# Kernel optimization log

Hardware: AMD Instinct MI355X
Metric: run time of the kernel (lower is better)

## Reference

```python
import jax, jax.numpy as jnp
import numpy as np

B, N, D, E, L = 8, 4096, 256, 65536, 1  # graphs, padded nodes, d_model, padded edges, num_layers


def setup_inputs() -> dict:
    key = jax.random.key(0)
    ks = jax.random.split(key, 9)
    x = jax.random.normal(ks[0], (B, N, D), dtype=jnp.float32)
    edge_index = jax.random.randint(ks[1], (B, 2, E), 0, N)
    edge_weight = jax.random.uniform(ks[2], (B, E), dtype=jnp.float32)
    mask = jax.random.randint(ks[3], (B, N), 0, 2).astype(jnp.int32)
    s = 1.0 / np.sqrt(D)
    # GatedGraphConv per-layer linear weight [L, D, D]
    W = jax.random.uniform(ks[4], (L, D, D), jnp.float32, -s, s)
    # GRUCell parameters (r, z, n stacked)
    W_ih = jax.random.uniform(ks[5], (3 * D, D), jnp.float32, -s, s)
    W_hh = jax.random.uniform(ks[6], (3 * D, D), jnp.float32, -s, s)
    b_ih = jax.random.uniform(ks[7], (3 * D,), jnp.float32, -s, s)
    b_hh = jax.random.uniform(ks[8], (3 * D,), jnp.float32, -s, s)
    return {"x": x, "edge_index": edge_index, "edge_weight": edge_weight,
            "mask": mask, "W": W, "W_ih": W_ih, "W_hh": W_hh,
            "b_ih": b_ih, "b_hh": b_hh}


def _gated_graph_conv(x, u, v, ew, W, W_ih, W_hh, b_ih, b_hh):
    """x:[B,N,D]; u,v:[B,E] src/dst indices; ew:[B,E] (already masked)."""
    h = x
    for l in range(L):
        m = jnp.einsum('bnd,de->bne', h, W[l])            # linear transform
        msg = jnp.take_along_axis(m, u[..., None], axis=1) * ew[..., None]  # [B,E,D]
        agg = jax.vmap(lambda ms, vi: jax.ops.segment_sum(ms, vi, num_segments=N))(msg, v)
        # GRUCell(input=agg, hidden=h)
        gi = agg @ W_ih.T + b_ih                          # [B,N,3D]
        gh = h @ W_hh.T + b_hh
        r = jax.nn.sigmoid(gi[..., :D] + gh[..., :D])
        z = jax.nn.sigmoid(gi[..., D:2 * D] + gh[..., D:2 * D])
        n = jnp.tanh(gi[..., 2 * D:] + r * gh[..., 2 * D:])
        h = (1.0 - z) * n + z * h
    return h


def reference(x, edge_index, edge_weight, mask, W, W_ih, W_hh, b_ih, b_hh):
    node_valid = mask > 0                                  # [B,N]
    u = edge_index[:, 0]                                   # source
    v = edge_index[:, 1]                                   # target
    # Drop edges touching invalid nodes: weight -> 0 (equivalent under sum aggr)
    e_valid = jnp.take_along_axis(node_valid, u, axis=1) & jnp.take_along_axis(node_valid, v, axis=1)
    ew = edge_weight * e_valid.astype(edge_weight.dtype)
    h = _gated_graph_conv(x, u, v, ew, W, W_ih, W_hh, b_ih, b_hh)
    # Invalid nodes stay zero (original writes only valid rows of a zeros output)
    return h * node_valid[..., None].astype(h.dtype)
```

## Files before the change

kernel.cpp:

```cpp
#include <hip/hip_runtime.h>
#include <math.h>

#define Bn 8
#define Nn 4096
#define Dn 256
#define En 65536
#define CAP 48

typedef __bf16 bf8 __attribute__((ext_vector_type(8)));
typedef float f4 __attribute__((ext_vector_type(4)));
typedef unsigned short us8 __attribute__((ext_vector_type(8)));

__device__ __forceinline__ float4 ld4(const float* p) { return *(const float4*)p; }

__device__ __forceinline__ unsigned short f2bf(float f) {
    union { float f; unsigned int u; } v; v.f = f;
    unsigned int r = v.u + 0x7fff + ((v.u >> 16) & 1);
    return (unsigned short)(r >> 16);
}
__device__ __forceinline__ float bf2f(unsigned short h) {
    union { unsigned int u; float f; } v; v.u = (unsigned int)h << 16;
    return v.f;
}


__device__ __forceinline__ void stage16c(const unsigned short* __restrict__ gchunk,
                                         int stride, char* ldschunk, int lane) {
    int u = lane >> 3, s = lane & 7;
    int xx = s ^ (u & 7);
    const unsigned short* g = gchunk + (size_t)(2 * u + (xx >> 2)) * stride + (xx & 3) * 8;
    __builtin_amdgcn_global_load_lds((const __attribute__((address_space(1))) void*)g,
                                     (__attribute__((address_space(3))) void*)ldschunk,
                                     16, 0, 0);
}

__device__ __forceinline__ bf8 fragld(const unsigned short* region, int r, int q) {
    int s = (((r & 1) << 2) | q) ^ ((r >> 1) & 7);
    return *(const bf8*)(region + (r >> 1) * 64 + s * 8);
}

__device__ __forceinline__ void ldswrite8(unsigned short* region, int r, int q,
                                          const unsigned short* vals) {
    int s = (((r & 1) << 2) | q) ^ ((r >> 1) & 7);
    *(us8*)(region + (r >> 1) * 64 + s * 8) = *(const us8*)vals;
}


__device__ void rowscan_piece(const int* __restrict__ mask, int* __restrict__ rowidx,
                              int* __restrict__ rowcnt, int* part) {
    int t = threadIdx.x;
    int base = t * 128;
    unsigned long long b0 = 0, b1 = 0;
    int s = 0;
#pragma unroll 8
    for (int i = 0; i < 64; i++) {
        int m = mask[base + i] > 0;
        b0 |= (unsigned long long)m << i; s += m;
    }
#pragma unroll 8
    for (int i = 0; i < 64; i++) {
        int m = mask[base + 64 + i] > 0;
        b1 |= (unsigned long long)m << i; s += m;
    }
    part[t] = s;
    __syncthreads();
    for (int st = 1; st < 256; st <<= 1) {
        int v = (t >= st) ? part[t - st] : 0;
        __syncthreads();
        part[t] += v;
        __syncthreads();
    }
    int run = part[t] - s;
    for (int i = 0; i < 64; i++)
        if ((b0 >> i) & 1) rowidx[run++] = base + i;
    for (int i = 0; i < 64; i++)
        if ((b1 >> i) & 1) rowidx[run++] = base + 64 + i;
    if ((t & 31) == 31) rowcnt[1 + (t >> 5)] = part[t];
    if (t == 255) rowcnt[0] = part[255];
}

__device__ void wf_piece(int wfi, const float* __restrict__ Wih, const float* __restrict__ W,
                         unsigned short* __restrict__ Ball, unsigned short* lds) {
    int t = threadIdx.x, lane = t & 63, w = t >> 6;
    int wr = w >> 1, wc = w & 1, q = lane >> 4, c16 = lane & 15;
    int o0 = (wfi % 6) * 128, d0b = (wfi / 6) * 64;
    f4 acc[4][2];
    f4 zz = {0.f, 0.f, 0.f, 0.f};
#pragma unroll
    for (int rt = 0; rt < 4; rt++)
#pragma unroll
        for (int ct = 0; ct < 2; ct++) acc[rt][ct] = zz;

    int r = t >> 1, half = t & 1;
    for (int k0 = 0; k0 < 256; k0 += 32) {
        const float* pa = Wih + (size_t)(o0 + r) * 256 + k0 + half * 16;
        float4 a0 = ld4(pa), a1 = ld4(pa + 4), a2 = ld4(pa + 8), a3 = ld4(pa + 12);
        float4 b0, b1, b2, b3;
        if (t < 128) {
            const float* pb = W + (size_t)(d0b + r) * 256 + k0 + half * 16;
            b0 = ld4(pb); b1 = ld4(pb + 4); b2 = ld4(pb + 8); b3 = ld4(pb + 12);
        }
        __syncthreads();
        unsigned short tmp[16];
        tmp[0] = f2bf(a0.x); tmp[1] = f2bf(a0.y); tmp[2] = f2bf(a0.z); tmp[3] = f2bf(a0.w);
        tmp[4] = f2bf(a1.x); tmp[5] = f2bf(a1.y); tmp[6] = f2bf(a1.z); tmp[7] = f2bf(a1.w);
        tmp[8] = f2bf(a2.x); tmp[9] = f2bf(a2.y); tmp[10] = f2bf(a2.z); tmp[11] = f2bf(a2.w);
        tmp[12] = f2bf(a3.x); tmp[13] = f2bf(a3.y); tmp[14] = f2bf(a3.z); tmp[15] = f2bf(a3.w);
        ldswrite8(lds, r, half * 2, tmp);
        ldswrite8(lds, r, half * 2 + 1, tmp + 8);
        if (t < 128) {
            unsigned short tb[16];
            tb[0] = f2bf(b0.x); tb[1] = f2bf(b0.y); tb[2] = f2bf(b0.z); tb[3] = f2bf(b0.w);
            tb[4] = f2bf(b1.x); tb[5] = f2bf(b1.y); tb[6] = f2bf(b1.z); tb[7] = f2bf(b1.w);
            tb[8] = f2bf(b2.x); tb[9] = f2bf(b2.y); tb[10] = f2bf(b2.z); tb[11] = f2bf(b2.w);
            tb[12] = f2bf(b3.x); tb[13] = f2bf(b3.y); tb[14] = f2bf(b3.z); tb[15] = f2bf(b3.w);
            ldswrite8(lds + 4096, r, half * 2, tb);
            ldswrite8(lds + 4096, r, half * 2 + 1, tb + 8);
        }
        __syncthreads();
        bf8 a[4];
#pragma unroll
        for (int rt = 0; rt < 4; rt++) a[rt] = fragld(lds, wr * 64 + rt * 16 + c16, q);
#pragma unroll
        for (int ct = 0; ct < 2; ct++) {
            bf8 b = fragld(lds + 4096, wc * 32 + ct * 16 + c16, q);
#pragma unroll
            for (int rt = 0; rt < 4; rt++)
                acc[rt][ct] = __builtin_amdgcn_mfma_f32_16x16x32_bf16(a[rt], b, acc[rt][ct], 0, 0, 0);
        }
    }
#pragma unroll
    for (int ct = 0; ct < 2; ct++) {
        int col = d0b + wc * 32 + ct * 16 + c16;
#pragma unroll
        for (int rt = 0; rt < 4; rt++) {
            int ob = o0 + wr * 64 + rt * 16 + q * 4;
#pragma unroll
            for (int i = 0; i < 4; i++)
                Ball[(size_t)(ob + i) * 512 + col] = f2bf(acc[rt][ct][i]);
        }
    }
}

__global__ __launch_bounds__(256) void setup_kernel(const int* __restrict__ ei,
                                                    const int* __restrict__ mask,
                                                    const float* __restrict__ Wih,
                                                    const float* __restrict__ W,
                                                    const float* __restrict__ Whh,
                                                    const float* __restrict__ ew,
                                                    int* __restrict__ cnt,
                                                    int2* __restrict__ bucket,
                                                    int* __restrict__ rowidx,
                                                    int* __restrict__ rowcnt,
                                                    unsigned short* __restrict__ Ball,
                                                    float* __restrict__ out) {
    __shared__ __align__(16) unsigned short lds[6144];
    int b = blockIdx.x, t = threadIdx.x;
    if (b == 0) {
        rowscan_piece(mask, rowidx, rowcnt, (int*)lds);
        return;
    }
    if (b < 25) {
        wf_piece(b - 1, Wih, W, Ball, lds);
        return;
    }
    if (b < 217) {
        int i = ((b - 25) * 256 + t) * 4;
        float4 wv = ld4(Whh + i);
        int o = i >> 8, d = i & 255;
        ushort4 ov;
        ov.x = f2bf(wv.x); ov.y = f2bf(wv.y); ov.z = f2bf(wv.z); ov.w = f2bf(wv.w);
        *(ushort4*)(Ball + (size_t)o * 512 + 256 + d) = ov;
        return;
    }
    if (b < 2265) {
        int idx = (b - 217) * 256 + t;
        int bb = idx >> 16, e = idx & 65535;
        const int* eb = ei + (size_t)bb * 2 * En;
        int u = eb[e];
        int v = eb[En + e];
        const int* mb = mask + bb * Nn;
        if (mb[u] > 0 && mb[v] > 0) {
            int pos = atomicAdd(&cnt[bb * Nn + v], 1);
            if (pos < CAP) {
                int2 pr;
                pr.x = u;
                pr.y = __float_as_int(ew[(size_t)bb * En + e]);
                bucket[(size_t)(bb * Nn + v) * CAP + pos] = pr;
            }
        }
        return;
    }
    {
        int zb = b - 2265;
        int r = zb * 8 + (t >> 5);
        if (mask[r] > 0) return;
        int col = (t & 31) * 8;
        float4 z = make_float4(0.f, 0.f, 0.f, 0.f);
        *(float4*)(out + (size_t)r * 256 + col) = z;
        *(float4*)(out + (size_t)r * 256 + col + 4) = z;
    }
}


__global__ __launch_bounds__(256) void agg_kernel(const float* __restrict__ x,
                                                  const int* __restrict__ cnt,
                                                  const int2* __restrict__ bucket,
                                                  const int* __restrict__ rowidx,
                                                  const int* __restrict__ rowcnt,
                                                  unsigned short* __restrict__ Ac) {
    int wave = threadIdx.x >> 6, lane = threadIdx.x & 63;
    int b = blockIdx.x & 7;
    int slot = blockIdx.x >> 3;
    int p0 = (b == 0) ? 0 : rowcnt[b];
    int p1 = rowcnt[b + 1];
    const int2* bkb = bucket + (size_t)b * Nn * CAP;
    const int* cntb = cnt + b * Nn;
    const float* Xb = x + (size_t)b * Nn * 256;
    for (int i = p0 + slot * 4 + wave; i < p1; i += 4 * 512) {
        int v = rowidx[i];
        int n = v & 4095;
        float4 xv = ld4(Xb + (size_t)n * 256 + lane * 4);
        int m = cntb[n];
        m = m < CAP ? m : CAP;
        const int2* bk = bkb + (size_t)n * CAP;
        float a0 = 0.f, a1 = 0.f, a2 = 0.f, a3 = 0.f;
        for (int j = 0; j < m; j += 8) {
            int u[8]; float wv[8];
#pragma unroll
            for (int k = 0; k < 8; k++) {
                int jj = j + k;
                bool ok = jj < m;
                int2 pr = bk[ok ? jj : 0];
                u[k] = pr.x;
                wv[k] = ok ? __int_as_float(pr.y) : 0.f;
            }
            float4 mv[8];
#pragma unroll
            for (int k = 0; k < 8; k++) mv[k] = ld4(Xb + (size_t)u[k] * 256 + lane * 4);
#pragma unroll
            for (int k = 0; k < 8; k++) {
                a0 += wv[k] * mv[k].x; a1 += wv[k] * mv[k].y;
                a2 += wv[k] * mv[k].z; a3 += wv[k] * mv[k].w;
            }
        }
        ushort4 o;
        o.x = f2bf(a0); o.y = f2bf(a1); o.z = f2bf(a2); o.w = f2bf(a3);
        *(ushort4*)(Ac + (size_t)i * 512 + lane * 4) = o;
        ushort4 xo;
        xo.x = f2bf(xv.x); xo.y = f2bf(xv.y); xo.z = f2bf(xv.z); xo.w = f2bf(xv.w);
        *(ushort4*)(Ac + (size_t)i * 512 + 256 + lane * 4) = xo;
    }
}


#define GRU_STAGE(kk, bufbase)                                                      \
    {                                                                               \
        if (w < 6) {                                                                \
            _Pragma("unroll") for (int j = 0; j < 2; j++) {                         \
                int c = w * 2 + j;                                                  \
                const unsigned short* src;                                          \
                if (c < 8)                                                          \
                    src = Ac + (size_t)(row0 + c * 16) * 512 + (kk) * 32;           \
                else {                                                              \
                    int idx = c - 8, g = idx >> 1, h = idx & 1;                     \
                    src = Ball + (size_t)(g * 256 + d0 + h * 16) * 512 + (kk) * 32; \
                }                                                                   \
                stage16c(src, 512, (char*)(bufbase) + c * 1024, lane);              \
            }                                                                       \
        } else {                                                                    \
            int c = 12 + (w - 6);                                                   \
            int idx = c - 8, g = idx >> 1, h = idx & 1;                             \
            const unsigned short* src =                                             \
                Ball + (size_t)(g * 256 + d0 + h * 16) * 512 + (kk) * 32;           \
            stage16c(src, 512, (char*)(bufbase) + c * 1024, lane);                  \
        }                                                                           \
    }

#define GRU_COMPUTE(bufbase, ACCM)                                                  \
    {                                                                               \
        const unsigned short* rb = (bufbase);                                       \
        bf8 a0 = fragld(rb + (wr * 2) * 512, c16, q);                               \
        bf8 a1 = fragld(rb + (wr * 2 + 1) * 512, c16, q);                           \
        bf8 br = fragld(rb + (8 + wc) * 512, c16, q);                               \
        bf8 bz = fragld(rb + (10 + wc) * 512, c16, q);                              \
        bf8 bm = fragld(rb + (12 + wc) * 512, c16, q);                              \
        acc_r[0] = __builtin_amdgcn_mfma_f32_16x16x32_bf16(a0, br, acc_r[0], 0, 0, 0); \
        acc_r[1] = __builtin_amdgcn_mfma_f32_16x16x32_bf16(a1, br, acc_r[1], 0, 0, 0); \
        acc_z[0] = __builtin_amdgcn_mfma_f32_16x16x32_bf16(a0, bz, acc_z[0], 0, 0, 0); \
        acc_z[1] = __builtin_amdgcn_mfma_f32_16x16x32_bf16(a1, bz, acc_z[1], 0, 0, 0); \
        ACCM[0] = __builtin_amdgcn_mfma_f32_16x16x32_bf16(a0, bm, ACCM[0], 0, 0, 0);   \
        ACCM[1] = __builtin_amdgcn_mfma_f32_16x16x32_bf16(a1, bm, ACCM[1], 0, 0, 0);   \
    }

#define GRU_WAITV(n05, n67)                                                         \
    if (w < 6) { asm volatile("s_waitcnt vmcnt(" #n05 ")" ::: "memory"); }          \
    else       { asm volatile("s_waitcnt vmcnt(" #n67 ")" ::: "memory"); }          \
    __builtin_amdgcn_sched_barrier(0);

#define GRU_STEP(kk, STAGEBUF, COMPBUF, ACCM)                                       \
    __builtin_amdgcn_s_barrier();             \
    GRU_STAGE((kk) + 2, STAGEBUF)                                                   \
    GRU_WAITV(4, 2)                                 \
    __builtin_amdgcn_s_barrier();                   \
    __builtin_amdgcn_s_setprio(1);                                                  \
    GRU_COMPUTE(COMPBUF, ACCM)                                                      \
    __builtin_amdgcn_s_setprio(0);                                                  \
    __builtin_amdgcn_sched_barrier(0);

#define GRU_STEP_LAST(kk, COMPBUF, ACCM, n05, n67)                                  \
    __builtin_amdgcn_s_barrier();                                                   \
    GRU_WAITV(n05, n67)                                                             \
    __builtin_amdgcn_s_barrier();                                                   \
    __builtin_amdgcn_s_setprio(1);                                                  \
    GRU_COMPUTE(COMPBUF, ACCM)                                                      \
    __builtin_amdgcn_s_setprio(0);                                                  \
    __builtin_amdgcn_sched_barrier(0);

__global__ __launch_bounds__(512, 6) void gru_kernel(const unsigned short* __restrict__ Ac,
                                                     const unsigned short* __restrict__ Ball,
                                                     const float* __restrict__ bih,
                                                     const float* __restrict__ bhh,
                                                     const int* __restrict__ rowidx,
                                                     const int* __restrict__ rowcnt,
                                                     float* __restrict__ out) {
    __shared__ __align__(16) unsigned short lds[21504];
    const int t = threadIdx.x;
    const int lane = t & 63, w = t >> 6;
    const int wr = w >> 1, wc = w & 1;
    const int q = lane >> 4, c16 = lane & 15;
    const int cnt = rowcnt[0];
    const int nact = (cnt + 127) >> 7;
    if (blockIdx.x >= nact) return;
    int q8 = nact >> 3, r8 = nact & 7;
    int xcd = blockIdx.x & 7, jj = blockIdx.x >> 3;
    int xp = (xcd < r8 ? xcd * (q8 + 1) : r8 * (q8 + 1) + (xcd - r8) * q8) + jj;
    const int row0 = xp * 128, d0 = blockIdx.y * 32;

    f4 acc_r[2], acc_z[2], acc_gn[2], acc_hn[2];
    f4 zz = {0.f, 0.f, 0.f, 0.f};
#pragma unroll
    for (int rt = 0; rt < 2; rt++) {
        acc_r[rt] = zz; acc_z[rt] = zz;
        acc_gn[rt] = zz; acc_hn[rt] = zz;
    }

    unsigned short* bufA = lds;
    unsigned short* bufB = lds + 7168;
    unsigned short* bufC = lds + 14336;

    GRU_STAGE(0, bufA)
    GRU_STAGE(1, bufB)

    GRU_STEP(0,  bufC, bufA, acc_gn)
    GRU_STEP(1,  bufA, bufB, acc_gn)
    GRU_STEP(2,  bufB, bufC, acc_gn)
    GRU_STEP(3,  bufC, bufA, acc_gn)
    GRU_STEP(4,  bufA, bufB, acc_gn)
    GRU_STEP(5,  bufB, bufC, acc_gn)
    GRU_STEP(6,  bufC, bufA, acc_gn)
    GRU_STEP(7,  bufA, bufB, acc_gn)
    GRU_STEP(8,  bufB, bufC, acc_hn)
    GRU_STEP(9,  bufC, bufA, acc_hn)
    GRU_STEP(10, bufA, bufB, acc_hn)
    GRU_STEP(11, bufB, bufC, acc_hn)
    GRU_STEP(12, bufC, bufA, acc_hn)
    GRU_STEP(13, bufA, bufB, acc_hn)
    GRU_STEP_LAST(14, bufC, acc_hn, 2, 1)
    GRU_STEP_LAST(15, bufA, acc_hn, 0, 0)

    {
        int dd = d0 + wc * 16 + c16;
        float b_r = bih[dd] + bhh[dd];
        float b_z = bih[dd + 256] + bhh[dd + 256];
        float b_gn = bih[dd + 512];
        float b_hn = bhh[dd + 512];
#pragma unroll
        for (int rt = 0; rt < 2; rt++) {
            int rbase = row0 + wr * 32 + rt * 16 + q * 4;
#pragma unroll
            for (int i = 0; i < 4; i++) {
                int rc = rbase + i;
                if (rc < cnt) {
                    float sr = acc_r[rt][i] + b_r;
                    float sz = acc_z[rt][i] + b_z;
                    float gn = acc_gn[rt][i] + b_gn;
                    float hn = acc_hn[rt][i] + b_hn;
                    float rg = 1.f / (1.f + __expf(-sr));
                    float zg = 1.f / (1.f + __expf(-sz));
                    float pre = gn + rg * hn;
                    float e2 = __expf(2.f * pre);
                    float ng = 1.f - 2.f / (e2 + 1.f);
                    float xv = bf2f(Ac[(size_t)rc * 512 + 256 + dd]);
                    float h = (1.f - zg) * ng + zg * xv;
                    int v = rowidx[rc];
                    out[(size_t)v * 256 + dd] = h;
                }
            }
        }
    }
}


extern "C" void kernel_launch(void* const* d_in, const int* in_sizes, int n_in,
                              void* d_out, int out_size, void* d_ws, size_t ws_size,
                              hipStream_t stream) {
    const float* x   = (const float*)d_in[0];
    const int*   ei  = (const int*)d_in[1];
    const float* ew  = (const float*)d_in[2];
    const int*   msk = (const int*)d_in[3];
    const float* W   = (const float*)d_in[4];
    const float* Wih = (const float*)d_in[5];
    const float* Whh = (const float*)d_in[6];
    const float* bih = (const float*)d_in[7];
    const float* bhh = (const float*)d_in[8];
    float* out = (float*)d_out;

    char* p = (char*)d_ws;
    unsigned short* Ac   = (unsigned short*)p; p += (size_t)Bn * Nn * 512 * 2;
    unsigned short* Ball = (unsigned short*)p; p += (size_t)768 * 512 * 2;
    int2* bucket = (int2*)p;  p += (size_t)Bn * Nn * CAP * sizeof(int2);
    int* cnt    = (int*)p;    p += (size_t)Bn * Nn * sizeof(int);
    int* rowidx = (int*)p;    p += (size_t)Bn * Nn * sizeof(int);
    int* rowcnt = (int*)p;    p += 128;

    hipMemsetAsync(cnt, 0, (size_t)Bn * Nn * sizeof(int), stream);
    setup_kernel<<<6361, 256, 0, stream>>>(ei, msk, Wih, W, Whh, ew, cnt, bucket,
                                           rowidx, rowcnt, Ball, out);
    agg_kernel<<<8 * 512, 256, 0, stream>>>(x, cnt, bucket, rowidx, rowcnt, Ac);
    gru_kernel<<<dim3(256, 8), 512, 0, stream>>>(Ac, Ball, bih, bhh, rowidx, rowcnt, out);
}
```

Before: 160.7 us.

## Split GRU GEMM staging into separate A and B pipelines with deeper B prefetch

The combined A/B triple-buffer staging in the GRU GEMM is replaced by separate pipelines. Waves 0-3 stage the activation tile three-deep, and waves 4-6 stage the weight tile four-deep, prefetching three k-steps ahead. The aim is to balance load issue across waves and hide more of the weight fetch latency. LDS use grows from 21504 to 24576 shorts, which may reduce occupancy at 6 blocks per CU, and the per-wave vmcnt accounting becomes more intricate.

```diff
diff --git a/kernel.cpp b/kernel.cpp
--- a/kernel.cpp
+++ b/kernel.cpp
@@ -254,37 +254,33 @@
 }
 
 
-#define GRU_STAGE(kk, bufbase)                                                      \
+#define STAGE_A(kk, abuf)                                                           \
     {                                                                               \
-        if (w < 6) {                                                                \
-            _Pragma("unroll") for (int j = 0; j < 2; j++) {                         \
-                int c = w * 2 + j;                                                  \
-                const unsigned short* src;                                          \
-                if (c < 8)                                                          \
-                    src = Ac + (size_t)(row0 + c * 16) * 512 + (kk) * 32;           \
-                else {                                                              \
-                    int idx = c - 8, g = idx >> 1, h = idx & 1;                     \
-                    src = Ball + (size_t)(g * 256 + d0 + h * 16) * 512 + (kk) * 32; \
-                }                                                                   \
-                stage16c(src, 512, (char*)(bufbase) + c * 1024, lane);              \
-            }                                                                       \
-        } else {                                                                    \
-            int c = 12 + (w - 6);                                                   \
-            int idx = c - 8, g = idx >> 1, h = idx & 1;                             \
+        _Pragma("unroll") for (int j = 0; j < 2; j++) {                             \
+            int c = w * 2 + j;                                                      \
+            const unsigned short* src = Ac + (size_t)(row0 + c * 16) * 512 + (kk) * 32; \
+            stage16c(src, 512, (char*)(abuf) + c * 1024, lane);                     \
+        }                                                                           \
+    }
+
+#define STAGE_B(kk, bbuf)                                                           \
+    {                                                                               \
+        _Pragma("unroll") for (int j = 0; j < 2; j++) {                             \
+            int c = (w - 4) * 2 + j;                                                \
+            int g = c >> 1, h = c & 1;                                              \
             const unsigned short* src =                                             \
                 Ball + (size_t)(g * 256 + d0 + h * 16) * 512 + (kk) * 32;           \
-            stage16c(src, 512, (char*)(bufbase) + c * 1024, lane);                  \
+            stage16c(src, 512, (char*)(bbuf) + c * 1024, lane);                     \
         }                                                                           \
     }
 
-#define GRU_COMPUTE(bufbase, ACCM)                                                  \
+#define GRU_COMPUTE(abuf, bbuf, ACCM)                                               \
     {                                                                               \
-        const unsigned short* rb = (bufbase);                                       \
-        bf8 a0 = fragld(rb + (wr * 2) * 512, c16, q);                               \
-        bf8 a1 = fragld(rb + (wr * 2 + 1) * 512, c16, q);                           \
-        bf8 br = fragld(rb + (8 + wc) * 512, c16, q);                               \
-        bf8 bz = fragld(rb + (10 + wc) * 512, c16, q);                              \
-        bf8 bm = fragld(rb + (12 + wc) * 512, c16, q);                              \
+        bf8 a0 = fragld((abuf) + (wr * 2) * 512, c16, q);                           \
+        bf8 a1 = fragld((abuf) + (wr * 2 + 1) * 512, c16, q);                       \
+        bf8 br = fragld((bbuf) + (0 + wc) * 512, c16, q);                           \
+        bf8 bz = fragld((bbuf) + (2 + wc) * 512, c16, q);                           \
+        bf8 bm = fragld((bbuf) + (4 + wc) * 512, c16, q);                           \
         acc_r[0] = __builtin_amdgcn_mfma_f32_16x16x32_bf16(a0, br, acc_r[0], 0, 0, 0); \
         acc_r[1] = __builtin_amdgcn_mfma_f32_16x16x32_bf16(a1, br, acc_r[1], 0, 0, 0); \
         acc_z[0] = __builtin_amdgcn_mfma_f32_16x16x32_bf16(a0, bz, acc_z[0], 0, 0, 0); \
@@ -293,27 +289,19 @@
         ACCM[1] = __builtin_amdgcn_mfma_f32_16x16x32_bf16(a1, bm, ACCM[1], 0, 0, 0);   \
     }
 
-#define GRU_WAITV(n05, n67)                                                         \
-    if (w < 6) { asm volatile("s_waitcnt vmcnt(" #n05 ")" ::: "memory"); }          \
-    else       { asm volatile("s_waitcnt vmcnt(" #n67 ")" ::: "memory"); }          \
-    __builtin_amdgcn_sched_barrier(0);
-
-#define GRU_STEP(kk, STAGEBUF, COMPBUF, ACCM)                                       \
-    __builtin_amdgcn_s_barrier();             \
-    GRU_STAGE((kk) + 2, STAGEBUF)                                                   \
-    GRU_WAITV(4, 2)                                 \
-    __builtin_amdgcn_s_barrier();                   \
-    __builtin_amdgcn_s_setprio(1);                                                  \
-    GRU_COMPUTE(COMPBUF, ACCM)                                                      \
-    __builtin_amdgcn_s_setprio(0);                                                  \
-    __builtin_amdgcn_sched_barrier(0);
-
-#define GRU_STEP_LAST(kk, COMPBUF, ACCM, n05, n67)                                  \
+#define GRU_STEP(kk, DA, AST, DB, BST, ACMP, BCMP, NA, NB, ACCM)                    \
     __builtin_amdgcn_s_barrier();                                                   \
-    GRU_WAITV(n05, n67)                                                             \
+    if (w < 4) {                                                                    \
+        if (DA) STAGE_A((kk) + 2, AST)                                              \
+        asm volatile("s_waitcnt vmcnt(" #NA ")" ::: "memory");                      \
+    } else if (w < 7) {                                                             \
+        if (DB) STAGE_B((kk) + 3, BST)                                              \
+        asm volatile("s_waitcnt vmcnt(" #NB ")" ::: "memory");                      \
+    }                                                                               \
+    __builtin_amdgcn_sched_barrier(0);                                              \
     __builtin_amdgcn_s_barrier();                                                   \
     __builtin_amdgcn_s_setprio(1);                                                  \
-    GRU_COMPUTE(COMPBUF, ACCM)                                                      \
+    GRU_COMPUTE(ACMP, BCMP, ACCM)                                                   \
     __builtin_amdgcn_s_setprio(0);                                                  \
     __builtin_amdgcn_sched_barrier(0);
 
@@ -324,7 +312,7 @@
                                                      const int* __restrict__ rowidx,
                                                      const int* __restrict__ rowcnt,
                                                      float* __restrict__ out) {
-    __shared__ __align__(16) unsigned short lds[21504];
+    __shared__ __align__(16) unsigned short lds[24576];
     const int t = threadIdx.x;
     const int lane = t & 63, w = t >> 6;
     const int wr = w >> 1, wc = w & 1;
@@ -345,29 +333,39 @@
         acc_gn[rt] = zz; acc_hn[rt] = zz;
     }
 
-    unsigned short* bufA = lds;
-    unsigned short* bufB = lds + 7168;
-    unsigned short* bufC = lds + 14336;
-
-    GRU_STAGE(0, bufA)
-    GRU_STAGE(1, bufB)
-
-    GRU_STEP(0,  bufC, bufA, acc_gn)
-    GRU_STEP(1,  bufA, bufB, acc_gn)
-    GRU_STEP(2,  bufB, bufC, acc_gn)
-    GRU_STEP(3,  bufC, bufA, acc_gn)
-    GRU_STEP(4,  bufA, bufB, acc_gn)
-    GRU_STEP(5,  bufB, bufC, acc_gn)
-    GRU_STEP(6,  bufC, bufA, acc_gn)
-    GRU_STEP(7,  bufA, bufB, acc_gn)
-    GRU_STEP(8,  bufB, bufC, acc_hn)
-    GRU_STEP(9,  bufC, bufA, acc_hn)
-    GRU_STEP(10, bufA, bufB, acc_hn)
-    GRU_STEP(11, bufB, bufC, acc_hn)
-    GRU_STEP(12, bufC, bufA, acc_hn)
-    GRU_STEP(13, bufA, bufB, acc_hn)
-    GRU_STEP_LAST(14, bufC, acc_hn, 2, 1)
-    GRU_STEP_LAST(15, bufA, acc_hn, 0, 0)
+    unsigned short* A0 = lds;
+    unsigned short* A1 = lds + 4096;
+    unsigned short* A2 = lds + 8192;
+    unsigned short* B0 = lds + 12288;
+    unsigned short* B1 = lds + 15360;
+    unsigned short* B2 = lds + 18432;
+    unsigned short* B3 = lds + 21504;
+
+    if (w < 4) {
+        STAGE_A(0, A0)
+        STAGE_A(1, A1)
+    } else if (w < 7) {
+        STAGE_B(0, B0)
+        STAGE_B(1, B1)
+        STAGE_B(2, B2)
+    }
+
+    GRU_STEP( 0,  1, A2, 1, B3,  A0,  B0,   4, 6, acc_gn)
+    GRU_STEP( 1,  1, A0, 1, B0,  A1,  B1,   4, 6, acc_gn)
+    GRU_STEP( 2,  1, A1, 1, B1,  A2,  B2,   4, 6, acc_gn)
+    GRU_STEP( 3,  1, A2, 1, B2,  A0,  B3,   4, 6, acc_gn)
+    GRU_STEP( 4,  1, A0, 1, B3,  A1,  B0,   4, 6, acc_gn)
+    GRU_STEP( 5,  1, A1, 1, B0,  A2,  B1,   4, 6, acc_gn)
+    GRU_STEP( 6,  1, A2, 1, B1,  A0,  B2,   4, 6, acc_gn)
+    GRU_STEP( 7,  1, A0, 1, B2,  A1,  B3,   4, 6, acc_gn)
+    GRU_STEP( 8,  1, A1, 1, B3,  A2,  B0,   4, 6, acc_hn)
+    GRU_STEP( 9,  1, A2, 1, B0,  A0,  B1,   4, 6, acc_hn)
+    GRU_STEP(10,  1, A0, 1, B1,  A1,  B2,   4, 6, acc_hn)
+    GRU_STEP(11,  1, A1, 1, B2,  A2,  B3,   4, 6, acc_hn)
+    GRU_STEP(12,  1, A2, 1, B3,  A0,  B0,   4, 6, acc_hn)
+    GRU_STEP(13,  1, A0, 0, B0,  A1,  B1,   4, 4, acc_hn)
+    GRU_STEP(14,  0, A0, 0, B0,  A2,  B2,   2, 2, acc_hn)
+    GRU_STEP(15,  0, A0, 0, B0,  A0,  B3,   0, 0, acc_hn)
 
     {
         int dd = d0 + wc * 16 + c16;
```

After: 161.7 us. About the same (+0.6%).
